# Performance work log

Hardware: AMD Instinct MI355X
Metric: run time of the kernel (lower is better)

Reference implementation:

```python
import jax, jax.numpy as jnp
import numpy as np

IN_F = 4096
OUT_F = 4096
RANK = 16
ALPHA = 16
SCALING = ALPHA / RANK  # 1.0


def setup_inputs() -> dict:
    key = jax.random.key(0)
    k_x, k_w, k_b, k_a = jax.random.split(key, 4)
    x = jax.random.normal(k_x, (4, 2048, IN_F), dtype=jnp.float32)
    # frozen base linear params
    W = jax.random.normal(k_w, (OUT_F, IN_F), dtype=jnp.float32) * (1.0 / np.sqrt(IN_F))
    b = jax.random.normal(k_b, (OUT_F,), dtype=jnp.float32) * 0.01
    # LoRA params: A kaiming-uniform-like, B zeros per initial_weights(); use small
    bound = np.sqrt(6.0 / IN_F)  # kaiming_uniform(a=sqrt(5)) bound approx
    lora_A = jax.random.uniform(k_a, (RANK, IN_F), dtype=jnp.float32, minval=-bound, maxval=bound)
    lora_B = jax.random.normal(jax.random.fold_in(key, 7), (OUT_F, RANK), dtype=jnp.float32) * 0.01
    lora_bias = jnp.zeros((OUT_F,), dtype=jnp.float32)
    return {"x": x, "W": W, "b": b, "lora_A": lora_A, "lora_B": lora_B, "lora_bias": lora_bias}


def reference(x, W, b, lora_A, lora_B, lora_bias):
    # Original: F.linear(x, W + scaling*B@A, bias=b + lora_bias); dropout is Identity (p=0).
    # Algebraically equivalent form avoiding the [out,in] delta materialization:
    # y = x@W^T + scaling * (x@A^T)@B^T + (b + lora_bias)
    base = jnp.einsum('bsi,oi->bso', x, W)
    low = jnp.einsum('bsr,or->bso', jnp.einsum('bsi,ri->bsr', x, lora_A), lora_B)
    return base + SCALING * low + (b + lora_bias)
```

## Files before the change

kernel.cpp:

```cpp
#include <hip/hip_runtime.h>
#include <hip/hip_bf16.h>
#include <stdint.h>


#define M_DIM 8192
#define N_DIM 4096
#define K_DIM 4096
#define NT    (K_DIM / 64)

typedef __attribute__((ext_vector_type(8))) short bf16x8;
typedef __attribute__((ext_vector_type(4))) float f32x4;

#define BARRIER() __builtin_amdgcn_s_barrier()
#define WAITV8() asm volatile("s_waitcnt vmcnt(8)" ::: "memory")
#define WAITV4() asm volatile("s_waitcnt vmcnt(4)" ::: "memory")
#define WAITV0() asm volatile("s_waitcnt vmcnt(0)" ::: "memory")
#define LGKM0()  asm volatile("s_waitcnt lgkmcnt(0)" ::: "memory")
#define LGKM8()  asm volatile("s_waitcnt lgkmcnt(8)" ::: "memory")
#define MEMFENCE() asm volatile("" ::: "memory")

static __device__ __forceinline__ unsigned short f2bf(float f) {
    unsigned int u = __builtin_bit_cast(unsigned int, f);
    unsigned int r = (u + 0x7fffu + ((u >> 16) & 1u)) >> 16;
    return (unsigned short)r;
}

#define CONVX_BLOCKS 8192
__global__ __launch_bounds__(512) void conv_xw_kernel(
    const float* __restrict__ x, unsigned short* __restrict__ xb,
    const float* __restrict__ W, const float* __restrict__ lA,
    const float* __restrict__ lB, unsigned short* __restrict__ Wb) {
    const int bid = blockIdx.x;
    if (bid < CONVX_BLOCKS) {
        size_t i = ((size_t)bid * 512 + threadIdx.x) * 8;
        float4 a = *(const float4*)(x + i);
        float4 c = *(const float4*)(x + i + 4);
        union { unsigned short us[8]; uint4 v; } u;
        u.us[0] = f2bf(a.x); u.us[1] = f2bf(a.y); u.us[2] = f2bf(a.z); u.us[3] = f2bf(a.w);
        u.us[4] = f2bf(c.x); u.us[5] = f2bf(c.y); u.us[6] = f2bf(c.z); u.us[7] = f2bf(c.w);
        *(uint4*)(xb + i) = u.v;
        return;
    }
    const int nb = (bid - CONVX_BLOCKS) * 4;
    const int k0 = threadIdx.x * 8;

    float acc[4][8];
#pragma unroll
    for (int r = 0; r < 4; ++r) {
        const float4* w4 = (const float4*)(W + (size_t)(nb + r) * K_DIM + k0);
        float4 v0 = w4[0], v1 = w4[1];
        acc[r][0] = v0.x; acc[r][1] = v0.y; acc[r][2] = v0.z; acc[r][3] = v0.w;
        acc[r][4] = v1.x; acc[r][5] = v1.y; acc[r][6] = v1.z; acc[r][7] = v1.w;
    }
    float brs[4][16];
#pragma unroll
    for (int r = 0; r < 4; ++r)
#pragma unroll
        for (int t = 0; t < 16; ++t) brs[r][t] = lB[(size_t)(nb + r) * 16 + t];

#pragma unroll
    for (int t = 0; t < 16; ++t) {
        const float4* a4 = (const float4*)(lA + (size_t)t * K_DIM + k0);
        float4 v0 = a4[0], v1 = a4[1];
        float av[8] = {v0.x, v0.y, v0.z, v0.w, v1.x, v1.y, v1.z, v1.w};
#pragma unroll
        for (int r = 0; r < 4; ++r)
#pragma unroll
            for (int j = 0; j < 8; ++j) acc[r][j] += brs[r][t] * av[j];
    }
#pragma unroll
    for (int r = 0; r < 4; ++r) {
        union { unsigned short us[8]; uint4 v; } u;
#pragma unroll
        for (int j = 0; j < 8; ++j) u.us[j] = f2bf(acc[r][j]);
        *(uint4*)(Wb + (size_t)(nb + r) * K_DIM + k0) = u.v;
    }
}

__global__ __launch_bounds__(512, 2) void gemm_kernel(
    const unsigned short* __restrict__ A,
    const unsigned short* __restrict__ B,
    const float* __restrict__ bvec, const float* __restrict__ lbvec,
    float* __restrict__ C) {
    const int tid = threadIdx.x;
    const int lane = tid & 63;
    const int wid = tid >> 6;
    const int wr = wid >> 2;
    const int wc = wid & 3;

    const int bid = blockIdx.x;
    const int ntile = (bid & 7) * 2 + ((bid >> 3) & 1);
    const int mtile = bid >> 4;
    const int m0 = mtile * 256, n0 = ntile * 256;

    __shared__ __align__(16) unsigned short ldsA[2 * 2 * 128 * 64];
    __shared__ __align__(16) unsigned short ldsB[2 * 2 * 128 * 64];

    const int lr8 = lane >> 3;
    const int cch = (lane & 7) ^ lr8;
    const unsigned short* aSb = A + (size_t)(m0 + lr8) * K_DIM + cch * 8;
    const unsigned short* bSb = B + (size_t)(n0 + lr8) * K_DIM + cch * 8;

    auto stageA = [&](int par_, int h, int kt) {
#pragma unroll
        for (int s = 0; s < 2; ++s) {
            const int j = wid * 2 + s;
            const unsigned short* g = aSb + (size_t)(h * 128 + j * 8) * K_DIM + kt * 64;
            __builtin_amdgcn_global_load_lds(
                (const __attribute__((address_space(1))) void*)g,
                (__attribute__((address_space(3))) void*)(ldsA + (par_ * 2 + h) * 8192 + j * 512),
                16, 0, 0);
        }
    };
    auto stageB = [&](int par_, int h, int kt) {
#pragma unroll
        for (int s = 0; s < 2; ++s) {
            const int j = wid * 2 + s;
            const unsigned short* g = bSb + (size_t)(h * 128 + j * 8) * K_DIM + kt * 64;
            __builtin_amdgcn_global_load_lds(
                (const __attribute__((address_space(1))) void*)g,
                (__attribute__((address_space(3))) void*)(ldsB + (par_ * 2 + h) * 8192 + j * 512),
                16, 0, 0);
        }
    };

    const int rowByte = (lane & 15) * 128;
    const int swz = (lane & 7) << 4;
    const int kc0 = (0 * 64 + (lane >> 4) * 16) ^ swz;
    const int kc1 = (1 * 64 + (lane >> 4) * 16) ^ swz;
    const int baseBoff = (wc & 1) * 4096;

    auto readA = [&](int par_, int mf, int kk) -> bf16x8 {
        const char* p = (const char*)(ldsA + (par_ * 2 + wr) * 8192 + mf * 1024) +
                        rowByte + (kk ? kc1 : kc0);
        return *(const bf16x8*)p;
    };
    auto readB = [&](int par_, int nf, int kk) -> bf16x8 {
        const char* p = (const char*)(ldsB + (par_ * 2 + (wc >> 1)) * 8192 + baseBoff + nf * 1024) +
                        rowByte + (kk ? kc1 : kc0);
        return *(const bf16x8*)p;
    };

    f32x4 acc[8][4] = {};
    bf16x8 a[4][2], b[4][2];

    auto mfmaQ = [&](int qm, int qn) {
#pragma unroll
        for (int i = 0; i < 4; ++i)
#pragma unroll
            for (int jn = 0; jn < 2; ++jn)
#pragma unroll
                for (int kk = 0; kk < 2; ++kk)
                    acc[qm * 4 + i][qn * 2 + jn] = __builtin_amdgcn_mfma_f32_16x16x32_bf16(
                        a[i][kk], b[qn * 2 + jn][kk], acc[qm * 4 + i][qn * 2 + jn], 0, 0, 0);
    };

    stageA(0, 0, 0); stageA(0, 1, 0); stageB(0, 0, 0); stageB(0, 1, 0);
    stageA(1, 0, 1); stageA(1, 1, 1); stageB(1, 0, 1); stageB(1, 1, 1);
    WAITV8();
    BARRIER();

#define KTILE(kt, par)                                                          \
    {                                                                           \
                                                                        \
        _Pragma("unroll") for (int i = 0; i < 4; ++i)                           \
            _Pragma("unroll") for (int kk = 0; kk < 2; ++kk)                    \
                a[i][kk] = readA(par, i, kk);                                    \
        _Pragma("unroll") for (int nf = 0; nf < 2; ++nf)                        \
            _Pragma("unroll") for (int kk = 0; kk < 2; ++kk)                    \
                b[nf][kk] = readB(par, nf, kk);                                  \
        if ((kt) >= 1 && (kt) + 1 < NT) stageA((par) ^ 1, 0, (kt) + 1);         \
        LGKM8();                                                                \
        MEMFENCE();                                                             \
        BARRIER();                                                              \
        LGKM0();                                                                \
        __builtin_amdgcn_s_setprio(1); mfmaQ(0, 0); __builtin_amdgcn_s_setprio(0); \
        BARRIER();                                                              \
                                                                        \
        _Pragma("unroll") for (int nf = 2; nf < 4; ++nf)                        \
            _Pragma("unroll") for (int kk = 0; kk < 2; ++kk)                    \
                b[nf][kk] = readB(par, nf, kk);                                  \
        if ((kt) >= 1 && (kt) + 1 < NT) stageA((par) ^ 1, 1, (kt) + 1);         \
        MEMFENCE();                                                             \
        BARRIER();                                                              \
        LGKM0();                                                                \
        __builtin_amdgcn_s_setprio(1); mfmaQ(0, 1); __builtin_amdgcn_s_setprio(0); \
        BARRIER();                                                              \
                  \
        _Pragma("unroll") for (int i = 0; i < 4; ++i)                           \
            _Pragma("unroll") for (int kk = 0; kk < 2; ++kk)                    \
                a[i][kk] = readA(par, 4 + i, kk);                                \
        if ((kt) + 2 < NT) stageB(par, 0, (kt) + 2);                            \
        MEMFENCE();                                                             \
        BARRIER();                                                              \
        LGKM0();                                                                \
        __builtin_amdgcn_s_setprio(1); mfmaQ(1, 0); __builtin_amdgcn_s_setprio(0); \
        BARRIER();                                                              \
              \
        if ((kt) + 2 < NT) { stageB(par, 1, (kt) + 2); WAITV4(); }              \
        else { WAITV0(); }                                                      \
        MEMFENCE();                                                             \
        BARRIER();                                                              \
        __builtin_amdgcn_s_setprio(1); mfmaQ(1, 1); __builtin_amdgcn_s_setprio(0); \
        BARRIER();                                                              \
    }

#pragma unroll 1
    for (int kt = 0; kt < NT; kt += 2) {
        KTILE(kt, 0);
        KTILE(kt + 1, 1);
    }
#undef KTILE

#pragma unroll
    for (int nf = 0; nf < 4; ++nf) {
        const int gc = n0 + wc * 64 + nf * 16 + (lane & 15);
        const float bv = bvec[gc] + lbvec[gc];
#pragma unroll
        for (int mf = 0; mf < 8; ++mf) {
            const int gr0 = m0 + wr * 128 + mf * 16 + (lane >> 4) * 4;
            f32x4 v = acc[mf][nf];
#pragma unroll
            for (int j = 0; j < 4; ++j)
                __builtin_nontemporal_store(v[j] + bv, &C[(size_t)(gr0 + j) * N_DIM + gc]);
        }
    }
}

__global__ __launch_bounds__(256) void naive_kernel(
    const float* __restrict__ x, const float* __restrict__ W,
    const float* __restrict__ b, const float* __restrict__ lA,
    const float* __restrict__ lB, const float* __restrict__ lb,
    float* __restrict__ out) {
    __shared__ float xs[K_DIM];
    __shared__ float ts[16];
    const int m = blockIdx.x;
    const int tid = threadIdx.x;
    for (int k = tid; k < K_DIM; k += 256) xs[k] = x[(size_t)m * K_DIM + k];
    if (tid < 16) ts[tid] = 0.f;
    __syncthreads();
    float part[16] = {};
    for (int k = tid * 16; k < tid * 16 + 16; ++k) {
        float xv = xs[k];
#pragma unroll
        for (int r = 0; r < 16; ++r) part[r] += xv * lA[(size_t)r * K_DIM + k];
    }
#pragma unroll
    for (int r = 0; r < 16; ++r) atomicAdd(&ts[r], part[r]);
    __syncthreads();
    const int n = blockIdx.y * 256 + tid;
    float acc = b[n] + lb[n];
#pragma unroll
    for (int r = 0; r < 16; ++r) acc += ts[r] * lB[(size_t)n * 16 + r];
    const float* wrow = W + (size_t)n * K_DIM;
    for (int k = 0; k < K_DIM; ++k) acc += xs[k] * wrow[k];
    out[(size_t)m * N_DIM + n] = acc;
}

extern "C" void kernel_launch(void* const* d_in, const int* in_sizes, int n_in,
                              void* d_out, int out_size, void* d_ws, size_t ws_size,
                              hipStream_t stream) {
    const float* x  = (const float*)d_in[0];
    const float* W  = (const float*)d_in[1];
    const float* b  = (const float*)d_in[2];
    const float* lA = (const float*)d_in[3];
    const float* lB = (const float*)d_in[4];
    const float* lb = (const float*)d_in[5];
    float* out = (float*)d_out;

    const size_t xb_bytes = (size_t)M_DIM * K_DIM * 2;
    const size_t wb_bytes = (size_t)N_DIM * K_DIM * 2;

    if (ws_size >= xb_bytes + wb_bytes) {
        unsigned short* xb = (unsigned short*)d_ws;
        unsigned short* wb = (unsigned short*)((char*)d_ws + xb_bytes);

        conv_xw_kernel<<<CONVX_BLOCKS + N_DIM / 4, 512, 0, stream>>>(
            x, xb, W, lA, lB, wb);

        gemm_kernel<<<(M_DIM / 256) * (N_DIM / 256), 512, 0, stream>>>(xb, wb, b, lb, out);
    } else {
        dim3 grid(M_DIM, N_DIM / 256);
        naive_kernel<<<grid, 256, 0, stream>>>(x, W, b, lA, lB, lb, out);
    }
}
```

Before: 308.0 us.

## Load B operand directly from global into registers instead of LDS staging

Removes the LDS staging buffer for the B (weight) tile and has each wave load its B fragments straight from global memory into registers, interleaved with the A pipeline and tracked by vmcnt waits. This halves LDS usage and removes the B LDS writes and reads. In exchange, B is no longer shared across waves that use the same columns, so global and L2 traffic for B rises. The loads are also less coalesced (16-byte per-lane reads spanning rows), and global latency is exposed more directly before the MFMAs.

New measurement: 468.0 us. 51.9% more time.

```diff
diff --git a/kernel.cpp b/kernel.cpp
--- a/kernel.cpp
+++ b/kernel.cpp
@@ -12,11 +12,10 @@
 typedef __attribute__((ext_vector_type(4))) float f32x4;
 
 #define BARRIER() __builtin_amdgcn_s_barrier()
-#define WAITV8() asm volatile("s_waitcnt vmcnt(8)" ::: "memory")
+#define WAITV6() asm volatile("s_waitcnt vmcnt(6)" ::: "memory")
 #define WAITV4() asm volatile("s_waitcnt vmcnt(4)" ::: "memory")
 #define WAITV0() asm volatile("s_waitcnt vmcnt(0)" ::: "memory")
 #define LGKM0()  asm volatile("s_waitcnt lgkmcnt(0)" ::: "memory")
-#define LGKM8()  asm volatile("s_waitcnt lgkmcnt(8)" ::: "memory")
 #define MEMFENCE() asm volatile("" ::: "memory")
 
 static __device__ __forceinline__ unsigned short f2bf(float f) {
@@ -94,12 +93,10 @@
     const int m0 = mtile * 256, n0 = ntile * 256;
 
     __shared__ __align__(16) unsigned short ldsA[2 * 2 * 128 * 64];
-    __shared__ __align__(16) unsigned short ldsB[2 * 2 * 128 * 64];
 
     const int lr8 = lane >> 3;
     const int cch = (lane & 7) ^ lr8;
     const unsigned short* aSb = A + (size_t)(m0 + lr8) * K_DIM + cch * 8;
-    const unsigned short* bSb = B + (size_t)(n0 + lr8) * K_DIM + cch * 8;
 
     auto stageA = [&](int par_, int h, int kt) {
 #pragma unroll
@@ -112,33 +109,22 @@
                 16, 0, 0);
         }
     };
-    auto stageB = [&](int par_, int h, int kt) {
-#pragma unroll
-        for (int s = 0; s < 2; ++s) {
-            const int j = wid * 2 + s;
-            const unsigned short* g = bSb + (size_t)(h * 128 + j * 8) * K_DIM + kt * 64;
-            __builtin_amdgcn_global_load_lds(
-                (const __attribute__((address_space(1))) void*)g,
-                (__attribute__((address_space(3))) void*)(ldsB + (par_ * 2 + h) * 8192 + j * 512),
-                16, 0, 0);
-        }
-    };
 
     const int rowByte = (lane & 15) * 128;
     const int swz = (lane & 7) << 4;
     const int kc0 = (0 * 64 + (lane >> 4) * 16) ^ swz;
     const int kc1 = (1 * 64 + (lane >> 4) * 16) ^ swz;
-    const int baseBoff = (wc & 1) * 4096;
 
     auto readA = [&](int par_, int mf, int kk) -> bf16x8 {
         const char* p = (const char*)(ldsA + (par_ * 2 + wr) * 8192 + mf * 1024) +
                         rowByte + (kk ? kc1 : kc0);
         return *(const bf16x8*)p;
     };
-    auto readB = [&](int par_, int nf, int kk) -> bf16x8 {
-        const char* p = (const char*)(ldsB + (par_ * 2 + (wc >> 1)) * 8192 + baseBoff + nf * 1024) +
-                        rowByte + (kk ? kc1 : kc0);
-        return *(const bf16x8*)p;
+
+    const unsigned short* bF = B + (size_t)(n0 + wc * 64 + (lane & 15)) * K_DIM +
+                               (lane >> 4) * 8;
+    auto loadB = [&](int nf, int kk, int kt) -> bf16x8 {
+        return *(const bf16x8*)(bF + (size_t)(nf * 16) * K_DIM + kt * 64 + kk * 32);
     };
 
     f32x4 acc[8][4] = {};
@@ -155,51 +141,55 @@
                         a[i][kk], b[qn * 2 + jn][kk], acc[qm * 4 + i][qn * 2 + jn], 0, 0, 0);
     };
 
-    stageA(0, 0, 0); stageA(0, 1, 0); stageB(0, 0, 0); stageB(0, 1, 0);
-    stageA(1, 0, 1); stageA(1, 1, 1); stageB(1, 0, 1); stageB(1, 1, 1);
-    WAITV8();
+    stageA(0, 0, 0); stageA(0, 1, 0);
+#pragma unroll
+    for (int nf = 0; nf < 2; ++nf)
+#pragma unroll
+        for (int kk = 0; kk < 2; ++kk) b[nf][kk] = loadB(nf, kk, 0);
+    MEMFENCE();
+    WAITV4();
     BARRIER();
 
 #define KTILE(kt, par)                                                          \
     {                                                                           \
                                                                         \
+        _Pragma("unroll") for (int nf = 2; nf < 4; ++nf)                        \
+            _Pragma("unroll") for (int kk = 0; kk < 2; ++kk)                    \
+                b[nf][kk] = loadB(nf, kk, kt);                                   \
         _Pragma("unroll") for (int i = 0; i < 4; ++i)                           \
             _Pragma("unroll") for (int kk = 0; kk < 2; ++kk)                    \
                 a[i][kk] = readA(par, i, kk);                                    \
-        _Pragma("unroll") for (int nf = 0; nf < 2; ++nf)                        \
-            _Pragma("unroll") for (int kk = 0; kk < 2; ++kk)                    \
-                b[nf][kk] = readB(par, nf, kk);                                  \
-        if ((kt) >= 1 && (kt) + 1 < NT) stageA((par) ^ 1, 0, (kt) + 1);         \
-        LGKM8();                                                                \
+        if ((kt) + 1 < NT) stageA((par) ^ 1, 0, (kt) + 1);                      \
         MEMFENCE();                                                             \
         BARRIER();                                                              \
         LGKM0();                                                                \
+        if ((kt) + 1 < NT) { WAITV6(); } else { WAITV4(); }                     \
         __builtin_amdgcn_s_setprio(1); mfmaQ(0, 0); __builtin_amdgcn_s_setprio(0); \
         BARRIER();                                                              \
                                                                         \
-        _Pragma("unroll") for (int nf = 2; nf < 4; ++nf)                        \
-            _Pragma("unroll") for (int kk = 0; kk < 2; ++kk)                    \
-                b[nf][kk] = readB(par, nf, kk);                                  \
-        if ((kt) >= 1 && (kt) + 1 < NT) stageA((par) ^ 1, 1, (kt) + 1);         \
+        if ((kt) + 1 < NT) stageA((par) ^ 1, 1, (kt) + 1);                      \
         MEMFENCE();                                                             \
         BARRIER();                                                              \
-        LGKM0();                                                                \
+        if ((kt) + 1 < NT) { WAITV4(); } else { WAITV0(); }                     \
         __builtin_amdgcn_s_setprio(1); mfmaQ(0, 1); __builtin_amdgcn_s_setprio(0); \
         BARRIER();                                                              \
-                  \
+                                                                        \
         _Pragma("unroll") for (int i = 0; i < 4; ++i)                           \
             _Pragma("unroll") for (int kk = 0; kk < 2; ++kk)                    \
                 a[i][kk] = readA(par, 4 + i, kk);                                \
-        if ((kt) + 2 < NT) stageB(par, 0, (kt) + 2);                            \
         MEMFENCE();                                                             \
         BARRIER();                                                              \
         LGKM0();                                                                \
         __builtin_amdgcn_s_setprio(1); mfmaQ(1, 0); __builtin_amdgcn_s_setprio(0); \
         BARRIER();                                                              \
-              \
-        if ((kt) + 2 < NT) { stageB(par, 1, (kt) + 2); WAITV4(); }              \
-        else { WAITV0(); }                                                      \
-        MEMFENCE();                                                             \
+            \
+        if ((kt) + 1 < NT) {                                                    \
+            _Pragma("unroll") for (int nf = 0; nf < 2; ++nf)                    \
+                _Pragma("unroll") for (int kk = 0; kk < 2; ++kk)                \
+                    b[nf][kk] = loadB(nf, kk, (kt) + 1);                         \
+            MEMFENCE();                                                         \
+            WAITV4();                                                           \
+        } else { WAITV0(); }                                                    \
         BARRIER();                                                              \
         __builtin_amdgcn_s_setprio(1); mfmaQ(1, 1); __builtin_amdgcn_s_setprio(0); \
         BARRIER();                                                              \
```
